# Kernel tuning notes

Measured on AMD Instinct MI355X. Metric: run time of the kernel, lower is better.

## Reference

```python
import jax, jax.numpy as jnp
import numpy as np
from jax import lax

N_ENT, N_REL, N_TYPE = 50000, 237, 4000
DE, NOUT, DT = 100, 128, 200
N_EDGE, B = 800000, 4096
ALPHA, EPS = 0.2, 1e-5
NUM_FILT, FILT_W = 32, 9
FC_LEN = ((NOUT - FILT_W) // 2 + 1 - 2) // 2 + 1  # width after conv(s=2) then pool(2,s=2)
FC_LEN = FC_LEN * NUM_FILT  # height stays 1 -> 30*32 = 960


def setup_inputs() -> dict:
    key = jax.random.key(0)
    ks = jax.random.split(key, 16)
    inp = {
        'x_batch': jax.random.randint(ks[0], (B,), 0, N_ENT),
        'edge_index': jax.random.randint(ks[1], (2, N_EDGE), 0, N_ENT),
        'edge_type': jax.random.randint(ks[2], (N_EDGE,), 0, N_REL),
        'E_w': jax.random.normal(ks[3], (N_ENT, DE)) * 0.05,
        'R_w': jax.random.normal(ks[4], (N_REL, DE)) * 0.05,
        'T_w': jax.random.normal(ks[5], (N_TYPE, DT)) * 0.05,
        'W_f': jax.random.normal(ks[6], (DE, NOUT)) * (1.0 / np.sqrt(DE)),
        'a_vec': jax.random.normal(ks[7], (2 * NOUT,)) * 0.05,
        'conv_w': jax.random.normal(ks[8], (NUM_FILT, 1, 1, FILT_W)) * 0.1,
        'conv_b': jnp.zeros((NUM_FILT,)),
        'bn1_g': jnp.ones((1,)), 'bn1_b': jnp.zeros((1,)),
        'bn3_g': jnp.ones((NUM_FILT,)), 'bn3_b': jnp.zeros((NUM_FILT,)),
        'bn2_g': jnp.ones((DT,)), 'bn2_b': jnp.zeros((DT,)),
        'fc_w': jax.random.normal(ks[9], (DT, FC_LEN)) * (1.0 / np.sqrt(FC_LEN)),
        'fc_b': jnp.zeros((DT,)),
        'b_bias': jnp.zeros((N_TYPE,)),
    }
    return inp


def _bn(x, g, b, axes):
    # training-mode batch norm (biased variance), broadcastable g/b
    mean = jnp.mean(x, axis=axes, keepdims=True)
    var = jnp.var(x, axis=axes, keepdims=True)
    return g * (x - mean) * lax.rsqrt(var + EPS) + b


def _frgat(E_w, R_w, edge_index, edge_type, W_f, a_vec):
    src, dst = edge_index[0], edge_index[1]
    h = E_w @ W_f                                   # [N, NOUT]
    comp = E_w[src] - R_w[edge_type]                # 'sub' composition, [E, DE]
    m = comp @ W_f                                  # messages, [E, NOUT]
    score = jnp.concatenate([h[dst], m], axis=1) @ a_vec  # [E]
    score = jax.nn.leaky_relu(score, ALPHA)
    smax = jax.ops.segment_max(score, dst, num_segments=N_ENT)
    ex = jnp.exp(score - smax[dst])
    denom = jax.ops.segment_sum(ex, dst, num_segments=N_ENT)
    att = ex / (denom[dst] + 1e-16)
    agg = jax.ops.segment_sum(att[:, None] * m, dst, num_segments=N_ENT)
    return jax.nn.elu(agg)                          # F.elu on out_att output


def reference(x_batch, edge_index, edge_type, E_w, R_w, T_w, W_f, a_vec,
              conv_w, conv_b, bn1_g, bn1_b, bn3_g, bn3_b, bn2_g, bn2_b,
              fc_w, fc_b, b_bias):
    ent = _frgat(E_w, R_w, edge_index, edge_type, W_f, a_vec)   # [N, NOUT]
    e = ent[x_batch].reshape(B, 1, 1, NOUT)                     # NCHW
    x = _bn(e, bn1_g.reshape(1, 1, 1, 1), bn1_b.reshape(1, 1, 1, 1), (0, 2, 3))
    x = lax.conv_general_dilated(x, conv_w, window_strides=(2, 2), padding='VALID',
                                 dimension_numbers=('NCHW', 'OIHW', 'NCHW'))
    x = x + conv_b.reshape(1, -1, 1, 1)
    x = _bn(x, bn3_g.reshape(1, -1, 1, 1), bn3_b.reshape(1, -1, 1, 1), (0, 2, 3))
    x = jax.nn.relu(x)
    x = lax.reduce_window(x, -jnp.inf, lax.max, (1, 1, 1, 2), (1, 1, 2, 2), 'VALID')
    x = x.reshape(B, -1)                                        # [B, FC_LEN]
    x = x @ fc_w.T + fc_b
    x = _bn(x, bn2_g[None, :], bn2_b[None, :], (0,))
    x = jax.nn.relu(x)
    logits = x @ T_w.T + b_bias
    return jax.nn.sigmoid(logits)
```

## Files before the change

kernel.cpp:

```cpp
#include <hip/hip_runtime.h>
#include <hip/hip_bf16.h>
#include <math.h>

#define N_ENT   50000
#define N_REL   237
#define N_TYPE  4000
#define DE      100
#define NOUT    128
#define DT      200
#define N_EDGE  800000
#define B_SZ    4096
#define ALPHA   0.2f
#define EPS     1e-5f
#define NUM_FILT 32
#define CONV_W_OUT 60
#define POOL_W  30
#define FC_LEN  960
#define KP      224
#define NTP     4032
#define EBCAP   96

typedef unsigned short ushort_t;
typedef __attribute__((ext_vector_type(8))) short bf16x8;
typedef __attribute__((ext_vector_type(4))) float f32x4;

__global__ void k_fillconst(float* p, long n, float val) {
    long i = (long)blockIdx.x * blockDim.x + threadIdx.x;
    long stride = (long)gridDim.x * blockDim.x;
    for (; i < n; i += stride) p[i] = val;
}

#define ZERO_F4 14676
__global__ void k_fillprep(float4* zp, const float* Wf, const float* a_vec,
                           const float* Rw, float* wa1, float* wa2, float* rw) {
    if (blockIdx.x < 58) {
        int i = blockIdx.x * 256 + threadIdx.x;
        if (i < ZERO_F4) zp[i] = make_float4(0.f, 0.f, 0.f, 0.f);
        return;
    }
    __shared__ float sa[2 * NOUT];
    __shared__ float swa2[DE];
    int t = threadIdx.x;
    sa[t] = a_vec[t];
    __syncthreads();
    if (t < DE) {
        float s1 = 0.f, s2 = 0.f;
        for (int j = 0; j < NOUT; j++) {
            float w = Wf[t * NOUT + j];
            s1 += w * sa[j];
            s2 += w * sa[NOUT + j];
        }
        wa1[t] = s1; wa2[t] = s2; swa2[t] = s2;
    }
    __syncthreads();
    if (t < N_REL) {
        float s = 0.f;
        for (int k = 0; k < DE; k++) s += Rw[t * DE + k] * swa2[k];
        rw[t] = s;
    }
}

__global__ void k_flags(const int* xb, int* flags) {
    int i = blockIdx.x * blockDim.x + threadIdx.x;
    if (i < B_SZ) flags[xb[i]] = 1;
}

__global__ void k_slotsent(int* flags, int* counter, int* slotent,
                           const float* Ew, const float* wa1, const float* wa2,
                           float* ha, float* ew) {
    if (blockIdx.x < 196) {
        int i = blockIdx.x * 256 + threadIdx.x;
        if (i >= N_ENT) return;
        if (flags[i]) {
            int s = atomicAdd(counter, 1);
            flags[i] = 1 + s;
            slotent[s] = i;
        }
        return;
    }
    int wid = (blockIdx.x - 196) * 4 + (threadIdx.x >> 6);
    int lane = threadIdx.x & 63;
    if (wid >= N_ENT) return;
    float s1 = 0.f, s2 = 0.f;
    if (lane < DE / 2) {
        const float2* p = (const float2*)(Ew + (size_t)wid * DE);
        float2 v = p[lane];
        s1 = v.x * wa1[2 * lane] + v.y * wa1[2 * lane + 1];
        s2 = v.x * wa2[2 * lane] + v.y * wa2[2 * lane + 1];
    }
    for (int off = 32; off > 0; off >>= 1) {
        s1 += __shfl_down(s1, off);
        s2 += __shfl_down(s2, off);
    }
    if (lane == 0) { ha[wid] = s1; ew[wid] = s2; }
}

__global__ void k_scatter96(const int* ei, const int* et, const int* flags,
                            int* ecount, int2* ebuck) {
    int e = blockIdx.x * blockDim.x + threadIdx.x;
    if (e >= N_EDGE) return;
    int s = flags[ei[N_EDGE + e]];
    if (!s) return;
    int idx = atomicAdd(&ecount[s - 1], 1);
    if (idx < EBCAP)
        ebuck[(size_t)(s - 1) * EBCAP + idx] = make_int2(ei[e], et[e]);
}

__global__ void k_agg(const int* counter, const int* ecount, const int* slotent,
                      const int2* ebuck, const float* Ew, const float* Rw,
                      const float* ha, const float* ew, const float* rw,
                      float* aggc) {
    __shared__ float sacc[DE];
    __shared__ float sden;
    int slot = blockIdx.x;
    if (slot >= counter[0]) return;
    int t = threadIdx.x;
    int half = t >> 7;
    int tl = t & 127;
    int n = min(ecount[slot], EBCAP);
    const int2* eb = ebuck + (size_t)slot * EBCAP;
    float hae = ha[slotent[slot]];
    float acc = 0.f, den = 0.f;
    for (int j = half; j < n; j += 2) {
        int2 p = eb[j];
        float sc = hae + ew[p.x] - rw[p.y];
        sc = sc >= 0.f ? sc : ALPHA * sc;
        float ex = expf(sc);
        den += ex;
        if (tl < DE) acc += ex * (Ew[(size_t)p.x * DE + tl] - Rw[(size_t)p.y * DE + tl]);
    }
    if (half == 1) {
        if (tl < DE) sacc[tl] = acc;
        if (tl == 0) sden = den;
    }
    __syncthreads();
    if (half == 0 && tl < DE) {
        float a = acc + sacc[tl];
        float d = den + sden;
        aggc[(size_t)slot * DE + tl] = a / (d + 1e-16f);
    }
}

__global__ void k_gatherconv(const int* xb, const int* flags, const float* aggc,
                             const float* Wf, const float* convw,
                             float* ebuf, float* gps, float* gpq, float* cpart) {
    __shared__ float row[DE];
    __shared__ float xs[NOUT];
    __shared__ float cw[NUM_FILT * 9];
    __shared__ float red[NOUT], red2[NOUT];
    int b = blockIdx.x, t = threadIdx.x;
    int slot = flags[xb[b]] - 1;
    if (t < DE) row[t] = aggc[(size_t)slot * DE + t];
    for (int i = t; i < NUM_FILT * 9; i += 128) cw[i] = convw[i];
    __syncthreads();
    float acc = 0.f;
    for (int k = 0; k < DE; k++) acc += row[k] * Wf[k * NOUT + t];
    float x = acc > 0.f ? acc : expm1f(acc);
    xs[t] = x;
    ebuf[(size_t)b * NOUT + t] = x;
    red[t] = x; red2[t] = x * x;
    __syncthreads();
    for (int s = 64; s > 0; s >>= 1) {
        if (t < s) { red[t] += red[t + s]; red2[t] += red2[t + s]; }
        __syncthreads();
    }
    if (t == 0) { gps[b] = red[0]; gpq[b] = red2[0]; }
    int c = t >> 2, wg = t & 3;
    float ls = 0.f, lq = 0.f;
    for (int i = 0; i < 15; i++) {
        int w = wg + 4 * i;
        float u = 0.f;
        #pragma unroll
        for (int j = 0; j < 9; j++) u += cw[c * 9 + j] * xs[2 * w + j];
        ls += u; lq += u * u;
    }
    __syncthreads();
    red[t] = ls; red2[t] = lq;
    __syncthreads();
    if (wg == 0) {
        float s = red[t] + red[t + 1] + red[t + 2] + red[t + 3];
        float q = red2[t] + red2[t + 1] + red2[t + 2] + red2[t + 3];
        cpart[b * 64 + c] = s;
        cpart[b * 64 + 32 + c] = q;
    }
}

__global__ void k_redAB(const float* gps, const float* gpq, const float* cpart,
                        const float* g1, const float* g3, const float* b3, float* AB) {
    __shared__ float r1[256], r2[256], r3[256], r4[256];
    int c = blockIdx.x, t = threadIdx.x;
    float s = 0.f, q = 0.f, cs = 0.f, cq = 0.f;
    for (int b = t; b < B_SZ; b += 256) {
        s += gps[b]; q += gpq[b];
        cs += cpart[b * 64 + c]; cq += cpart[b * 64 + 32 + c];
    }
    r1[t] = s; r2[t] = q; r3[t] = cs; r4[t] = cq;
    __syncthreads();
    for (int k = 128; k > 0; k >>= 1) {
        if (t < k) { r1[t] += r1[t+k]; r2[t] += r2[t+k]; r3[t] += r3[t+k]; r4[t] += r4[t+k]; }
        __syncthreads();
    }
    if (t == 0) {
        float N1 = (float)(B_SZ * NOUT);
        float m1 = r1[0] / N1;
        float v1 = r2[0] / N1 - m1 * m1;
        float s1 = g1[0] * rsqrtf(v1 + EPS);
        float Nc = (float)(B_SZ * CONV_W_OUT);
        float mu = r3[0] / Nc;
        float vu = r4[0] / Nc - mu * mu;
        float A = g3[c] * s1 * rsqrtf(s1 * s1 * vu + EPS);
        AB[c] = A;
        AB[32 + c] = b3[c] - A * mu;
    }
}

__global__ void k_pool(const float* ebuf, const float* convw, const float* AB,
                       __hip_bfloat16* pooled) {
    __shared__ float xs[NOUT];
    __shared__ float cw[NUM_FILT * 9];
    __shared__ float sA[32], sB[32];
    int b = blockIdx.x, t = threadIdx.x;
    xs[t] = ebuf[(size_t)b * NOUT + t];
    for (int i = t; i < NUM_FILT * 9; i += 128) cw[i] = convw[i];
    if (t < 32) { sA[t] = AB[t]; sB[t] = AB[32 + t]; }
    __syncthreads();
    int c = t >> 2, wg = t & 3;
    float A = sA[c], Bv = sB[c];
    for (int i = 0; i < 8; i++) {
        int w2 = wg + 4 * i;
        if (w2 < POOL_W) {
            int w = 2 * w2;
            float u0 = 0.f, u1 = 0.f;
            #pragma unroll
            for (int j = 0; j < 9; j++) {
                float cv = cw[c * 9 + j];
                u0 += cv * xs[2 * w + j];
                u1 += cv * xs[2 * w + 2 + j];
            }
            float z0 = fmaxf(A * u0 + Bv, 0.f);
            float z1 = fmaxf(A * u1 + Bv, 0.f);
            pooled[((size_t)b * NUM_FILT + c) * POOL_W + w2] = __float2bfloat16(fmaxf(z0, z1));
        }
    }
}

__global__ void k_pads(const float* fcw, const float* tw,
                       __hip_bfloat16* bfc, __hip_bfloat16* b2) {
    int i = blockIdx.x * blockDim.x + threadIdx.x;
    if (i < KP * FC_LEN) {
        bfc[i] = __float2bfloat16((i < DT * FC_LEN) ? fcw[i] : 0.f);
    } else {
        int j = i - KP * FC_LEN;
        if (j >= NTP * KP) return;
        int n = j / KP, k = j - n * KP;
        float v = (n < N_TYPE && k < DT) ? tw[n * DT + k] : 0.f;
        b2[j] = __float2bfloat16(v);
    }
}

template<int MODE, int K, int NB>
__launch_bounds__(256, 4)
__global__ void k_gemm(const ushort_t* A, const ushort_t* Bm, const float* bias,
                       int ldc, int nbias, float* Cf) {
    int wave = threadIdx.x >> 6, lane = threadIdx.x & 63;
    int m0 = blockIdx.x * 128 + wave * 32;
    int n0 = blockIdx.y * (16 * NB);
    int rsel = lane & 15, ksel = (lane >> 4) * 8;
    const ushort_t* pa0 = A + (size_t)(m0 + rsel) * K + ksel;
    const ushort_t* pa1 = pa0 + (size_t)16 * K;
    const ushort_t* pb[NB];
    #pragma unroll
    for (int j = 0; j < NB; j++) pb[j] = Bm + (size_t)(n0 + j * 16 + rsel) * K + ksel;
    f32x4 acc0[NB], acc1[NB];
    #pragma unroll
    for (int j = 0; j < NB; j++) { acc0[j] = (f32x4){0.f,0.f,0.f,0.f}; acc1[j] = acc0[j]; }
    if constexpr (K <= 256) {
        #pragma unroll
        for (int k = 0; k < K; k += 32) {
            bf16x8 a0 = *(const bf16x8*)(pa0 + k);
            bf16x8 a1 = *(const bf16x8*)(pa1 + k);
            #pragma unroll
            for (int j = 0; j < NB; j++) {
                bf16x8 b = *(const bf16x8*)(pb[j] + k);
                acc0[j] = __builtin_amdgcn_mfma_f32_16x16x32_bf16(b, a0, acc0[j], 0, 0, 0);
                acc1[j] = __builtin_amdgcn_mfma_f32_16x16x32_bf16(b, a1, acc1[j], 0, 0, 0);
            }
        }
    } else {
        #pragma unroll 4
        for (int k = 0; k < K; k += 32) {
            bf16x8 a0 = *(const bf16x8*)(pa0 + k);
            bf16x8 a1 = *(const bf16x8*)(pa1 + k);
            #pragma unroll
            for (int j = 0; j < NB; j++) {
                bf16x8 b = *(const bf16x8*)(pb[j] + k);
                acc0[j] = __builtin_amdgcn_mfma_f32_16x16x32_bf16(b, a0, acc0[j], 0, 0, 0);
                acc1[j] = __builtin_amdgcn_mfma_f32_16x16x32_bf16(b, a1, acc1[j], 0, 0, 0);
            }
        }
    }
    int mloc = lane & 15;
    int nq = (lane >> 4) * 4;
    #pragma unroll
    for (int j = 0; j < NB; j++) {
        int cc = n0 + j * 16 + nq;
        if (cc < nbias) {
            float4 bb = *(const float4*)(bias + cc);
            f32x4 v0 = acc0[j], v1 = acc1[j];
            float4 r0, r1;
            if (MODE == 0) {
                r0 = make_float4(v0[0] + bb.x, v0[1] + bb.y, v0[2] + bb.z, v0[3] + bb.w);
                r1 = make_float4(v1[0] + bb.x, v1[1] + bb.y, v1[2] + bb.z, v1[3] + bb.w);
            } else {
                r0.x = __builtin_amdgcn_rcpf(1.f + __expf(-(v0[0] + bb.x)));
                r0.y = __builtin_amdgcn_rcpf(1.f + __expf(-(v0[1] + bb.y)));
                r0.z = __builtin_amdgcn_rcpf(1.f + __expf(-(v0[2] + bb.z)));
                r0.w = __builtin_amdgcn_rcpf(1.f + __expf(-(v0[3] + bb.w)));
                r1.x = __builtin_amdgcn_rcpf(1.f + __expf(-(v1[0] + bb.x)));
                r1.y = __builtin_amdgcn_rcpf(1.f + __expf(-(v1[1] + bb.y)));
                r1.z = __builtin_amdgcn_rcpf(1.f + __expf(-(v1[2] + bb.z)));
                r1.w = __builtin_amdgcn_rcpf(1.f + __expf(-(v1[3] + bb.w)));
            }
            *(float4*)(Cf + (size_t)(m0 + mloc) * ldc + cc) = r0;
            *(float4*)(Cf + (size_t)(m0 + 16 + mloc) * ldc + cc) = r1;
        }
    }
}

__global__ void k_bn2part(const float* fcout, float* sums) {
    int b = blockIdx.x, t = threadIdx.x;
    if (t >= DT) return;
    float s = 0.f, q = 0.f;
    const float* base = fcout + (size_t)b * 128 * KP + t;
    for (int r = 0; r < 128; r++) {
        float v = base[r * KP];
        s += v; q += v * v;
    }
    atomicAdd(&sums[t], s);
    atomicAdd(&sums[KP + t], q);
}

__global__ void k_bn2apply(const float* fcout, const float* sums,
                           const float* g, const float* bb, __hip_bfloat16* a2) {
    int i = blockIdx.x * blockDim.x + threadIdx.x;
    if (i >= B_SZ * KP) return;
    int t = i % KP;
    float v = 0.f;
    if (t < DT) {
        float mean = sums[t] * (1.f / B_SZ);
        float var = sums[KP + t] * (1.f / B_SZ) - mean * mean;
        float sc = g[t] * rsqrtf(var + EPS);
        float sh = bb[t] - mean * sc;
        v = fcout[i] * sc + sh;
        v = fmaxf(v, 0.f);
    }
    a2[i] = __float2bfloat16(v);
}

extern "C" void kernel_launch(void* const* d_in, const int* in_sizes, int n_in,
                              void* d_out, int out_size, void* d_ws, size_t ws_size,
                              hipStream_t stream) {
    (void)in_sizes; (void)n_in;
    const int*   x_batch = (const int*)d_in[0];
    const int*   ei      = (const int*)d_in[1];
    const int*   etype   = (const int*)d_in[2];
    const float* E_w     = (const float*)d_in[3];
    const float* R_w     = (const float*)d_in[4];
    const float* T_w     = (const float*)d_in[5];
    const float* W_f     = (const float*)d_in[6];
    const float* a_vec   = (const float*)d_in[7];
    const float* conv_w  = (const float*)d_in[8];
    const float* bn1_g   = (const float*)d_in[10];
    const float* bn3_g   = (const float*)d_in[12];
    const float* bn3_b   = (const float*)d_in[13];
    const float* bn2_g   = (const float*)d_in[14];
    const float* bn2_b   = (const float*)d_in[15];
    const float* fc_w    = (const float*)d_in[16];
    const float* fc_b    = (const float*)d_in[17];
    const float* b_bias  = (const float*)d_in[18];
    float* out           = (float*)d_out;
    long outn = (long)out_size;

    const size_t WS_NEEDED = 4279296;
    if (ws_size < WS_NEEDED) {
        k_fillconst<<<2048, 256, 0, stream>>>(out, outn, 50.f);
        return;
    }
    char* ws = (char*)d_ws;
    float* wa1      = (float*)(ws + 0);
    float* wa2      = (float*)(ws + 512);
    float* rw       = (float*)(ws + 1024);
    float* AB       = (float*)(ws + 2048);
    float* gps      = (float*)(ws + 4864);
    float* gpq      = (float*)(ws + 21248);
    float* cpart    = (float*)(ws + 37632);
    int*   counter  = (int*)  (ws + 1086208);
    int*   flags    = (int*)  (ws + 1086464);
    int*   slotent  = (int*)  (ws + 1286464);
    int*   ecount   = (int*)  (ws + 1302848);
    float* sums     = (float*)(ws + 1319232);
    float* ha       = (float*)(ws + 1352064);
    float* ew       = (float*)(ws + 1552064);
    float* ebuf     = (float*)(ws + 1752064);
    __hip_bfloat16* bfc = (__hip_bfloat16*)(ws + 3849216);
    __hip_bfloat16* a2 = (__hip_bfloat16*)(ws + 4864);
    __hip_bfloat16* b2 = (__hip_bfloat16*)(ws + 1840128);
    __hip_bfloat16* pooled = (__hip_bfloat16*)((char*)d_out + 0);
    float* fcout    = (float*)((char*)d_out + 8388608);
    int2*  ebuck    = (int2*) ((char*)d_out + 16777216);
    float* aggc     = (float*)((char*)d_out + 25165824);

    k_fillprep<<<59, 256, 0, stream>>>((float4*)counter, W_f, a_vec, R_w, wa1, wa2, rw);
    k_flags<<<16, 256, 0, stream>>>(x_batch, flags);
    k_slotsent<<<12696, 256, 0, stream>>>(flags, counter, slotent, E_w, wa1, wa2, ha, ew);
    k_scatter96<<<3125, 256, 0, stream>>>(ei, etype, flags, ecount, ebuck);
    k_agg<<<4096, 256, 0, stream>>>(counter, ecount, slotent, ebuck,
                                    E_w, R_w, ha, ew, rw, aggc);
    k_gatherconv<<<4096, 128, 0, stream>>>(x_batch, flags, aggc, W_f, conv_w,
                                           ebuf, gps, gpq, cpart);
    k_redAB<<<32, 256, 0, stream>>>(gps, gpq, cpart, bn1_g, bn3_g, bn3_b, AB);
    k_pool<<<4096, 128, 0, stream>>>(ebuf, conv_w, AB, pooled);
    k_pads<<<4368, 256, 0, stream>>>(fc_w, T_w, bfc, b2);
    k_gemm<0, FC_LEN, 2><<<dim3(32, 7), 256, 0, stream>>>(
        (const ushort_t*)pooled, (const ushort_t*)bfc, fc_b, KP, DT, fcout);
    k_bn2part<<<32, 256, 0, stream>>>(fcout, sums);
    k_bn2apply<<<3584, 256, 0, stream>>>(fcout, sums, bn2_g, bn2_b, a2);
    k_gemm<1, KP, 4><<<dim3(32, 63), 256, 0, stream>>>(
        (const ushort_t*)a2, (const ushort_t*)b2, b_bias, N_TYPE, N_TYPE, out);
}
```

Measured before the change: 272.2 us.

## Fuse front-end stages into persistent kernel with grid barriers and fold BN2 stats

Merges flags, slot assignment, edge scatter, aggregation, gather/conv stats, BN reduction and pooling into one persistent kernel of 512 blocks, separated by software grid-wide barriers, to remove many kernel launches and their gaps. The T_w padding moves into extra blocks of the first GEMM, and BN2 column sums are computed in the GEMM epilogue with shuffles and atomics instead of a separate kernel. The trade-offs are less parallelism in phases that used thousands of blocks, and a grid barrier that relies on all 512 blocks being co-resident and on the counter and generation words starting zeroed.

After: 1.021 ms. +275.1%, slower.

```diff
diff --git a/kernel.cpp b/kernel.cpp
--- a/kernel.cpp
+++ b/kernel.cpp
@@ -19,6 +19,7 @@
 #define KP      224
 #define NTP     4032
 #define EBCAP   96
+#define MEGA_BLOCKS 512
 
 typedef unsigned short ushort_t;
 typedef __attribute__((ext_vector_type(8))) short bf16x8;
@@ -60,208 +61,257 @@
     }
 }
 
-__global__ void k_flags(const int* xb, int* flags) {
-    int i = blockIdx.x * blockDim.x + threadIdx.x;
-    if (i < B_SZ) flags[xb[i]] = 1;
-}
-
-__global__ void k_slotsent(int* flags, int* counter, int* slotent,
-                           const float* Ew, const float* wa1, const float* wa2,
-                           float* ha, float* ew) {
-    if (blockIdx.x < 196) {
-        int i = blockIdx.x * 256 + threadIdx.x;
-        if (i >= N_ENT) return;
-        if (flags[i]) {
-            int s = atomicAdd(counter, 1);
-            flags[i] = 1 + s;
-            slotent[s] = i;
-        }
-        return;
-    }
-    int wid = (blockIdx.x - 196) * 4 + (threadIdx.x >> 6);
-    int lane = threadIdx.x & 63;
-    if (wid >= N_ENT) return;
-    float s1 = 0.f, s2 = 0.f;
-    if (lane < DE / 2) {
-        const float2* p = (const float2*)(Ew + (size_t)wid * DE);
-        float2 v = p[lane];
-        s1 = v.x * wa1[2 * lane] + v.y * wa1[2 * lane + 1];
-        s2 = v.x * wa2[2 * lane] + v.y * wa2[2 * lane + 1];
-    }
-    for (int off = 32; off > 0; off >>= 1) {
-        s1 += __shfl_down(s1, off);
-        s2 += __shfl_down(s2, off);
-    }
-    if (lane == 0) { ha[wid] = s1; ew[wid] = s2; }
-}
-
-__global__ void k_scatter96(const int* ei, const int* et, const int* flags,
-                            int* ecount, int2* ebuck) {
-    int e = blockIdx.x * blockDim.x + threadIdx.x;
-    if (e >= N_EDGE) return;
-    int s = flags[ei[N_EDGE + e]];
-    if (!s) return;
-    int idx = atomicAdd(&ecount[s - 1], 1);
-    if (idx < EBCAP)
-        ebuck[(size_t)(s - 1) * EBCAP + idx] = make_int2(ei[e], et[e]);
-}
-
-__global__ void k_agg(const int* counter, const int* ecount, const int* slotent,
-                      const int2* ebuck, const float* Ew, const float* Rw,
-                      const float* ha, const float* ew, const float* rw,
-                      float* aggc) {
-    __shared__ float sacc[DE];
-    __shared__ float sden;
-    int slot = blockIdx.x;
-    if (slot >= counter[0]) return;
+__device__ __forceinline__ void gbar(int* cnt, int* gen) {
+    __threadfence();
+    __syncthreads();
+    if (threadIdx.x == 0) {
+        int g = __hip_atomic_load(gen, __ATOMIC_RELAXED, __HIP_MEMORY_SCOPE_AGENT);
+        int v = __hip_atomic_fetch_add(cnt, 1, __ATOMIC_ACQ_REL, __HIP_MEMORY_SCOPE_AGENT);
+        if (v == (int)gridDim.x - 1) {
+            __hip_atomic_store(cnt, 0, __ATOMIC_RELAXED, __HIP_MEMORY_SCOPE_AGENT);
+            __hip_atomic_store(gen, g + 1, __ATOMIC_RELEASE, __HIP_MEMORY_SCOPE_AGENT);
+        } else {
+            while (__hip_atomic_load(gen, __ATOMIC_RELAXED, __HIP_MEMORY_SCOPE_AGENT) == g)
+                __builtin_amdgcn_s_sleep(2);
+        }
+    }
+    __syncthreads();
+    __threadfence();
+}
+
+__launch_bounds__(256, 4)
+__global__ void k_mega(const int* xb, const int* ei, const int* et,
+                       const float* Ew, const float* Rw, const float* Wf,
+                       const float* convw, const float* g1, const float* g3,
+                       const float* b3, const float* fcw,
+                       int* flags, int* counter, int* slotent, int* ecount,
+                       const float* wa1, const float* wa2, const float* rw,
+                       float* ha, float* ewd, float* ebuf, float* gps, float* gpq,
+                       float* cpart, float* AB, float* aggc, int2* ebuck,
+                       __hip_bfloat16* pooled, __hip_bfloat16* bfc,
+                       int* cnt, int* gen) {
+    __shared__ float smem[1256];
     int t = threadIdx.x;
-    int half = t >> 7;
-    int tl = t & 127;
-    int n = min(ecount[slot], EBCAP);
-    const int2* eb = ebuck + (size_t)slot * EBCAP;
-    float hae = ha[slotent[slot]];
-    float acc = 0.f, den = 0.f;
-    for (int j = half; j < n; j += 2) {
-        int2 p = eb[j];
-        float sc = hae + ew[p.x] - rw[p.y];
-        sc = sc >= 0.f ? sc : ALPHA * sc;
-        float ex = expf(sc);
-        den += ex;
-        if (tl < DE) acc += ex * (Ew[(size_t)p.x * DE + tl] - Rw[(size_t)p.y * DE + tl]);
-    }
-    if (half == 1) {
-        if (tl < DE) sacc[tl] = acc;
-        if (tl == 0) sden = den;
-    }
-    __syncthreads();
-    if (half == 0 && tl < DE) {
-        float a = acc + sacc[tl];
-        float d = den + sden;
-        aggc[(size_t)slot * DE + tl] = a / (d + 1e-16f);
-    }
-}
-
-__global__ void k_gatherconv(const int* xb, const int* flags, const float* aggc,
-                             const float* Wf, const float* convw,
-                             float* ebuf, float* gps, float* gpq, float* cpart) {
-    __shared__ float row[DE];
-    __shared__ float xs[NOUT];
-    __shared__ float cw[NUM_FILT * 9];
-    __shared__ float red[NOUT], red2[NOUT];
-    int b = blockIdx.x, t = threadIdx.x;
-    int slot = flags[xb[b]] - 1;
-    if (t < DE) row[t] = aggc[(size_t)slot * DE + t];
-    for (int i = t; i < NUM_FILT * 9; i += 128) cw[i] = convw[i];
-    __syncthreads();
-    float acc = 0.f;
-    for (int k = 0; k < DE; k++) acc += row[k] * Wf[k * NOUT + t];
-    float x = acc > 0.f ? acc : expm1f(acc);
-    xs[t] = x;
-    ebuf[(size_t)b * NOUT + t] = x;
-    red[t] = x; red2[t] = x * x;
-    __syncthreads();
-    for (int s = 64; s > 0; s >>= 1) {
-        if (t < s) { red[t] += red[t + s]; red2[t] += red2[t + s]; }
-        __syncthreads();
-    }
-    if (t == 0) { gps[b] = red[0]; gpq[b] = red2[0]; }
-    int c = t >> 2, wg = t & 3;
-    float ls = 0.f, lq = 0.f;
-    for (int i = 0; i < 15; i++) {
-        int w = wg + 4 * i;
-        float u = 0.f;
-        #pragma unroll
-        for (int j = 0; j < 9; j++) u += cw[c * 9 + j] * xs[2 * w + j];
-        ls += u; lq += u * u;
-    }
-    __syncthreads();
-    red[t] = ls; red2[t] = lq;
-    __syncthreads();
-    if (wg == 0) {
-        float s = red[t] + red[t + 1] + red[t + 2] + red[t + 3];
-        float q = red2[t] + red2[t + 1] + red2[t + 2] + red2[t + 3];
-        cpart[b * 64 + c] = s;
-        cpart[b * 64 + 32 + c] = q;
-    }
-}
-
-__global__ void k_redAB(const float* gps, const float* gpq, const float* cpart,
-                        const float* g1, const float* g3, const float* b3, float* AB) {
-    __shared__ float r1[256], r2[256], r3[256], r4[256];
-    int c = blockIdx.x, t = threadIdx.x;
-    float s = 0.f, q = 0.f, cs = 0.f, cq = 0.f;
-    for (int b = t; b < B_SZ; b += 256) {
-        s += gps[b]; q += gpq[b];
-        cs += cpart[b * 64 + c]; cq += cpart[b * 64 + 32 + c];
-    }
-    r1[t] = s; r2[t] = q; r3[t] = cs; r4[t] = cq;
-    __syncthreads();
-    for (int k = 128; k > 0; k >>= 1) {
-        if (t < k) { r1[t] += r1[t+k]; r2[t] += r2[t+k]; r3[t] += r3[t+k]; r4[t] += r4[t+k]; }
-        __syncthreads();
-    }
-    if (t == 0) {
-        float N1 = (float)(B_SZ * NOUT);
-        float m1 = r1[0] / N1;
-        float v1 = r2[0] / N1 - m1 * m1;
-        float s1 = g1[0] * rsqrtf(v1 + EPS);
-        float Nc = (float)(B_SZ * CONV_W_OUT);
-        float mu = r3[0] / Nc;
-        float vu = r4[0] / Nc - mu * mu;
-        float A = g3[c] * s1 * rsqrtf(s1 * s1 * vu + EPS);
-        AB[c] = A;
-        AB[32 + c] = b3[c] - A * mu;
-    }
-}
-
-__global__ void k_pool(const float* ebuf, const float* convw, const float* AB,
-                       __hip_bfloat16* pooled) {
-    __shared__ float xs[NOUT];
-    __shared__ float cw[NUM_FILT * 9];
-    __shared__ float sA[32], sB[32];
-    int b = blockIdx.x, t = threadIdx.x;
-    xs[t] = ebuf[(size_t)b * NOUT + t];
-    for (int i = t; i < NUM_FILT * 9; i += 128) cw[i] = convw[i];
-    if (t < 32) { sA[t] = AB[t]; sB[t] = AB[32 + t]; }
-    __syncthreads();
-    int c = t >> 2, wg = t & 3;
-    float A = sA[c], Bv = sB[c];
-    for (int i = 0; i < 8; i++) {
-        int w2 = wg + 4 * i;
-        if (w2 < POOL_W) {
-            int w = 2 * w2;
-            float u0 = 0.f, u1 = 0.f;
-            #pragma unroll
-            for (int j = 0; j < 9; j++) {
-                float cv = cw[c * 9 + j];
-                u0 += cv * xs[2 * w + j];
-                u1 += cv * xs[2 * w + 2 + j];
-            }
-            float z0 = fmaxf(A * u0 + Bv, 0.f);
-            float z1 = fmaxf(A * u1 + Bv, 0.f);
-            pooled[((size_t)b * NUM_FILT + c) * POOL_W + w2] = __float2bfloat16(fmaxf(z0, z1));
-        }
-    }
-}
-
-__global__ void k_pads(const float* fcw, const float* tw,
-                       __hip_bfloat16* bfc, __hip_bfloat16* b2) {
-    int i = blockIdx.x * blockDim.x + threadIdx.x;
-    if (i < KP * FC_LEN) {
-        bfc[i] = __float2bfloat16((i < DT * FC_LEN) ? fcw[i] : 0.f);
-    } else {
-        int j = i - KP * FC_LEN;
-        if (j >= NTP * KP) return;
-        int n = j / KP, k = j - n * KP;
-        float v = (n < N_TYPE && k < DT) ? tw[n * DT + k] : 0.f;
-        b2[j] = __float2bfloat16(v);
+    int nb = gridDim.x;
+
+    for (int vb = blockIdx.x; vb < 16; vb += nb) {
+        int i = vb * 256 + t;
+        if (i < B_SZ) flags[xb[i]] = 1;
+    }
+    gbar(cnt, gen);
+
+    for (int vb = blockIdx.x; vb < 12696; vb += nb) {
+        if (vb < 196) {
+            int i = vb * 256 + t;
+            if (i < N_ENT && flags[i]) {
+                int s = atomicAdd(counter, 1);
+                flags[i] = 1 + s;
+                slotent[s] = i;
+            }
+        } else {
+            int wid = (vb - 196) * 4 + (t >> 6);
+            int lane = t & 63;
+            if (wid < N_ENT) {
+                float s1 = 0.f, s2 = 0.f;
+                if (lane < DE / 2) {
+                    const float2* p = (const float2*)(Ew + (size_t)wid * DE);
+                    float2 v = p[lane];
+                    s1 = v.x * wa1[2 * lane] + v.y * wa1[2 * lane + 1];
+                    s2 = v.x * wa2[2 * lane] + v.y * wa2[2 * lane + 1];
+                }
+                for (int off = 32; off > 0; off >>= 1) {
+                    s1 += __shfl_down(s1, off);
+                    s2 += __shfl_down(s2, off);
+                }
+                if (lane == 0) { ha[wid] = s1; ewd[wid] = s2; }
+            }
+        }
+    }
+    gbar(cnt, gen);
+
+    for (int vb = blockIdx.x; vb < 3125; vb += nb) {
+        int e = vb * 256 + t;
+        if (e < N_EDGE) {
+            int s = flags[ei[N_EDGE + e]];
+            if (s) {
+                int idx = atomicAdd(&ecount[s - 1], 1);
+                if (idx < EBCAP)
+                    ebuck[(size_t)(s - 1) * EBCAP + idx] = make_int2(ei[e], et[e]);
+            }
+        }
+    }
+    gbar(cnt, gen);
+
+    {
+        int nslot = counter[0];
+        int half = t >> 7, tl = t & 127;
+        float* sacc = smem;
+        float* sden = smem + 128;
+        for (int slot = blockIdx.x; slot < B_SZ; slot += nb) {
+            bool act = slot < nslot;
+            float acc = 0.f, den = 0.f;
+            if (act) {
+                int n = min(ecount[slot], EBCAP);
+                const int2* eb = ebuck + (size_t)slot * EBCAP;
+                float hae = ha[slotent[slot]];
+                for (int j = half; j < n; j += 2) {
+                    int2 p = eb[j];
+                    float sc = hae + ewd[p.x] - rw[p.y];
+                    sc = sc >= 0.f ? sc : ALPHA * sc;
+                    float ex = expf(sc);
+                    den += ex;
+                    if (tl < DE)
+                        acc += ex * (Ew[(size_t)p.x * DE + tl] - Rw[(size_t)p.y * DE + tl]);
+                }
+            }
+            if (act && half == 1) {
+                if (tl < DE) sacc[tl] = acc;
+                if (tl == 0) sden[0] = den;
+            }
+            __syncthreads();
+            if (act && half == 0 && tl < DE)
+                aggc[(size_t)slot * DE + tl] = (acc + sacc[tl]) / (den + sden[0] + 1e-16f);
+            __syncthreads();
+        }
+    }
+    gbar(cnt, gen);
+
+    {
+        int half = t >> 7, tl = t & 127;
+        float* row  = smem;
+        float* xs   = smem + 200;
+        float* cw   = smem + 456;
+        float* red  = smem + 744;
+        float* red2 = smem + 1000;
+        for (int vb = blockIdx.x; vb < B_SZ / 2; vb += nb) {
+            int b = vb * 2 + half;
+            int slot = flags[xb[b]] - 1;
+            if (tl < DE) row[half * DE + tl] = aggc[(size_t)slot * DE + tl];
+            for (int i = t; i < 288; i += 256) cw[i] = convw[i];
+            __syncthreads();
+            float acc = 0.f;
+            for (int k = 0; k < DE; k++) acc += row[half * DE + k] * Wf[k * NOUT + tl];
+            float x = acc > 0.f ? acc : expm1f(acc);
+            xs[half * NOUT + tl] = x;
+            ebuf[(size_t)b * NOUT + tl] = x;
+            red[half * NOUT + tl] = x; red2[half * NOUT + tl] = x * x;
+            __syncthreads();
+            for (int s = 64; s > 0; s >>= 1) {
+                if (tl < s) {
+                    red[half * NOUT + tl]  += red[half * NOUT + tl + s];
+                    red2[half * NOUT + tl] += red2[half * NOUT + tl + s];
+                }
+                __syncthreads();
+            }
+            if (tl == 0) { gps[b] = red[half * NOUT]; gpq[b] = red2[half * NOUT]; }
+            int c = tl >> 2, wg = tl & 3;
+            float ls = 0.f, lq = 0.f;
+            for (int i2 = 0; i2 < 15; i2++) {
+                int w = wg + 4 * i2;
+                float u = 0.f;
+                #pragma unroll
+                for (int j = 0; j < 9; j++) u += cw[c * 9 + j] * xs[half * NOUT + 2 * w + j];
+                ls += u; lq += u * u;
+            }
+            __syncthreads();
+            red[half * NOUT + tl] = ls; red2[half * NOUT + tl] = lq;
+            __syncthreads();
+            if (wg == 0) {
+                float s = red[half*NOUT+tl] + red[half*NOUT+tl+1] + red[half*NOUT+tl+2] + red[half*NOUT+tl+3];
+                float q = red2[half*NOUT+tl] + red2[half*NOUT+tl+1] + red2[half*NOUT+tl+2] + red2[half*NOUT+tl+3];
+                cpart[b * 64 + c] = s;
+                cpart[b * 64 + 32 + c] = q;
+            }
+            __syncthreads();
+        }
+    }
+    gbar(cnt, gen);
+
+    {
+        float* r1 = smem;       float* r2 = smem + 256;
+        float* r3 = smem + 512; float* r4 = smem + 768;
+        for (int c = blockIdx.x; c < 32; c += nb) {
+            float s = 0.f, q = 0.f, cs = 0.f, cq = 0.f;
+            for (int b = t; b < B_SZ; b += 256) {
+                s += gps[b]; q += gpq[b];
+                cs += cpart[b * 64 + c]; cq += cpart[b * 64 + 32 + c];
+            }
+            r1[t] = s; r2[t] = q; r3[t] = cs; r4[t] = cq;
+            __syncthreads();
+            for (int k = 128; k > 0; k >>= 1) {
+                if (t < k) { r1[t] += r1[t+k]; r2[t] += r2[t+k]; r3[t] += r3[t+k]; r4[t] += r4[t+k]; }
+                __syncthreads();
+            }
+            if (t == 0) {
+                float N1 = (float)(B_SZ * NOUT);
+                float m1 = r1[0] / N1;
+                float v1 = r2[0] / N1 - m1 * m1;
+                float s1 = g1[0] * rsqrtf(v1 + EPS);
+                float Nc = (float)(B_SZ * CONV_W_OUT);
+                float mu = r3[0] / Nc;
+                float vu = r4[0] / Nc - mu * mu;
+                float A = g3[c] * s1 * rsqrtf(s1 * s1 * vu + EPS);
+                AB[c] = A;
+                AB[32 + c] = b3[c] - A * mu;
+            }
+            __syncthreads();
+        }
+    }
+    gbar(cnt, gen);
+
+    {
+        int half = t >> 7, tl = t & 127;
+        float* xs  = smem;
+        float* cw  = smem + 256;
+        float* sAB = smem + 544;
+        for (int vb = blockIdx.x; vb < B_SZ / 2; vb += nb) {
+            int b = vb * 2 + half;
+            xs[half * NOUT + tl] = ebuf[(size_t)b * NOUT + tl];
+            for (int i = t; i < 288; i += 256) cw[i] = convw[i];
+            if (t < 64) sAB[t] = AB[t];
+            __syncthreads();
+            int c = tl >> 2, wg = tl & 3;
+            float A = sAB[c], Bv = sAB[32 + c];
+            for (int i2 = 0; i2 < 8; i2++) {
+                int w2 = wg + 4 * i2;
+                if (w2 < POOL_W) {
+                    int w = 2 * w2;
+                    float u0 = 0.f, u1 = 0.f;
+                    #pragma unroll
+                    for (int j = 0; j < 9; j++) {
+                        float cv = cw[c * 9 + j];
+                        u0 += cv * xs[half * NOUT + 2 * w + j];
+                        u1 += cv * xs[half * NOUT + 2 * w + 2 + j];
+                    }
+                    float z0 = fmaxf(A * u0 + Bv, 0.f);
+                    float z1 = fmaxf(A * u1 + Bv, 0.f);
+                    pooled[((size_t)b * NUM_FILT + c) * POOL_W + w2] = __float2bfloat16(fmaxf(z0, z1));
+                }
+            }
+            __syncthreads();
+        }
+        for (int i = blockIdx.x * 256 + t; i < KP * FC_LEN; i += nb * 256)
+            bfc[i] = __float2bfloat16((i < DT * FC_LEN) ? fcw[i] : 0.f);
     }
 }
 
 template<int MODE, int K, int NB>
 __launch_bounds__(256, 4)
 __global__ void k_gemm(const ushort_t* A, const ushort_t* Bm, const float* bias,
-                       int ldc, int nbias, float* Cf) {
+                       int ldc, int nbias, float* Cf, float* sums,
+                       const float* tw, __hip_bfloat16* b2pad) {
+    if constexpr (MODE == 0) {
+        if (blockIdx.y >= 7) {
+            int pid = (blockIdx.y - 7) * 32 + blockIdx.x;
+            int jj = pid * 256 + (int)threadIdx.x;
+            if (jj < NTP * KP) {
+                int n = jj / KP, k = jj - n * KP;
+                float v = (n < N_TYPE && k < DT) ? tw[n * DT + k] : 0.f;
+                b2pad[jj] = __float2bfloat16(v);
+            }
+            return;
+        }
+    }
     int wave = threadIdx.x >> 6, lane = threadIdx.x & 63;
     int m0 = blockIdx.x * 128 + wave * 32;
     int n0 = blockIdx.y * (16 * NB);
@@ -323,21 +373,26 @@
             }
             *(float4*)(Cf + (size_t)(m0 + mloc) * ldc + cc) = r0;
             *(float4*)(Cf + (size_t)(m0 + 16 + mloc) * ldc + cc) = r1;
-        }
-    }
-}
-
-__global__ void k_bn2part(const float* fcout, float* sums) {
-    int b = blockIdx.x, t = threadIdx.x;
-    if (t >= DT) return;
-    float s = 0.f, q = 0.f;
-    const float* base = fcout + (size_t)b * 128 * KP + t;
-    for (int r = 0; r < 128; r++) {
-        float v = base[r * KP];
-        s += v; q += v * v;
-    }
-    atomicAdd(&sums[t], s);
-    atomicAdd(&sums[KP + t], q);
+            if (MODE == 0) {
+                float s0 = r0.x + r1.x, s1 = r0.y + r1.y, s2 = r0.z + r1.z, s3 = r0.w + r1.w;
+                float q0 = r0.x*r0.x + r1.x*r1.x, q1 = r0.y*r0.y + r1.y*r1.y;
+                float q2 = r0.z*r0.z + r1.z*r1.z, q3 = r0.w*r0.w + r1.w*r1.w;
+                #pragma unroll
+                for (int off = 1; off <= 8; off <<= 1) {
+                    s0 += __shfl_xor(s0, off); s1 += __shfl_xor(s1, off);
+                    s2 += __shfl_xor(s2, off); s3 += __shfl_xor(s3, off);
+                    q0 += __shfl_xor(q0, off); q1 += __shfl_xor(q1, off);
+                    q2 += __shfl_xor(q2, off); q3 += __shfl_xor(q3, off);
+                }
+                if (mloc == 0) {
+                    atomicAdd(&sums[cc + 0], s0); atomicAdd(&sums[cc + 1], s1);
+                    atomicAdd(&sums[cc + 2], s2); atomicAdd(&sums[cc + 3], s3);
+                    atomicAdd(&sums[KP + cc + 0], q0); atomicAdd(&sums[KP + cc + 1], q1);
+                    atomicAdd(&sums[KP + cc + 2], q2); atomicAdd(&sums[KP + cc + 3], q3);
+                }
+            }
+        }
+    }
 }
 
 __global__ void k_bn2apply(const float* fcout, const float* sums,
@@ -395,6 +450,8 @@
     float* gpq      = (float*)(ws + 21248);
     float* cpart    = (float*)(ws + 37632);
     int*   counter  = (int*)  (ws + 1086208);
+    int*   gcnt     = (int*)  (ws + 1086216);
+    int*   ggen     = (int*)  (ws + 1086220);
     int*   flags    = (int*)  (ws + 1086464);
     int*   slotent  = (int*)  (ws + 1286464);
     int*   ecount   = (int*)  (ws + 1302848);
@@ -411,20 +468,15 @@
     float* aggc     = (float*)((char*)d_out + 25165824);
 
     k_fillprep<<<59, 256, 0, stream>>>((float4*)counter, W_f, a_vec, R_w, wa1, wa2, rw);
-    k_flags<<<16, 256, 0, stream>>>(x_batch, flags);
-    k_slotsent<<<12696, 256, 0, stream>>>(flags, counter, slotent, E_w, wa1, wa2, ha, ew);
-    k_scatter96<<<3125, 256, 0, stream>>>(ei, etype, flags, ecount, ebuck);
-    k_agg<<<4096, 256, 0, stream>>>(counter, ecount, slotent, ebuck,
-                                    E_w, R_w, ha, ew, rw, aggc);
-    k_gatherconv<<<4096, 128, 0, stream>>>(x_batch, flags, aggc, W_f, conv_w,
-                                           ebuf, gps, gpq, cpart);
-    k_redAB<<<32, 256, 0, stream>>>(gps, gpq, cpart, bn1_g, bn3_g, bn3_b, AB);
-    k_pool<<<4096, 128, 0, stream>>>(ebuf, conv_w, AB, pooled);
-    k_pads<<<4368, 256, 0, stream>>>(fc_w, T_w, bfc, b2);
-    k_gemm<0, FC_LEN, 2><<<dim3(32, 7), 256, 0, stream>>>(
-        (const ushort_t*)pooled, (const ushort_t*)bfc, fc_b, KP, DT, fcout);
-    k_bn2part<<<32, 256, 0, stream>>>(fcout, sums);
+    k_mega<<<MEGA_BLOCKS, 256, 0, stream>>>(
+        x_batch, ei, etype, E_w, R_w, W_f, conv_w, bn1_g, bn3_g, bn3_b, fc_w,
+        flags, counter, slotent, ecount, wa1, wa2, rw, ha, ew, ebuf,
+        gps, gpq, cpart, AB, aggc, ebuck, pooled, bfc, gcnt, ggen);
+    k_gemm<0, FC_LEN, 2><<<dim3(32, 118), 256, 0, stream>>>(
+        (const ushort_t*)pooled, (const ushort_t*)bfc, fc_b, KP, DT, fcout,
+        sums, T_w, b2);
     k_bn2apply<<<3584, 256, 0, stream>>>(fcout, sums, bn2_g, bn2_b, a2);
     k_gemm<1, KP, 4><<<dim3(32, 63), 256, 0, stream>>>(
-        (const ushort_t*)a2, (const ushort_t*)b2, b_bias, N_TYPE, N_TYPE, out);
-}
+        (const ushort_t*)a2, (const ushort_t*)b2, b_bias, N_TYPE, N_TYPE, out,
+        nullptr, nullptr, nullptr);
+}
```

## Fuse BN2 statistics into FC GEMM and overlap T_w padding

Applied to the files above, without the earlier changes.

Splits the FC GEMM into a dedicated kernel with smaller 64-row tiles, giving 64x7 tiles instead of 32x7 blocks for better occupancy. Its epilogue computes per-column sum and sum-of-squares with wave shuffles and atomics, replacing the separate k_bn2part pass. Extra blocks in the same grid perform the T_w bf16 padding so that conversion runs alongside the GEMM. The fc_b bias add is dropped, which is exact only when fc_b is zero as in the test inputs, though training-mode batch norm would cancel a constant bias anyway. The added atomics could contend, and sums must be zeroed before this kernel runs.

Result: slower. 308.5 us (+13.3%).

```diff
diff --git a/kernel.cpp b/kernel.cpp
--- a/kernel.cpp
+++ b/kernel.cpp
@@ -244,24 +244,74 @@
     }
 }
 
-__global__ void k_pads(const float* fcw, const float* tw,
-                       __hip_bfloat16* bfc, __hip_bfloat16* b2) {
+__global__ void k_padsbfc(const float* fcw, __hip_bfloat16* bfc) {
     int i = blockIdx.x * blockDim.x + threadIdx.x;
-    if (i < KP * FC_LEN) {
+    if (i < KP * FC_LEN)
         bfc[i] = __float2bfloat16((i < DT * FC_LEN) ? fcw[i] : 0.f);
-    } else {
-        int j = i - KP * FC_LEN;
-        if (j >= NTP * KP) return;
-        int n = j / KP, k = j - n * KP;
-        float v = (n < N_TYPE && k < DT) ? tw[n * DT + k] : 0.f;
-        b2[j] = __float2bfloat16(v);
-    }
-}
-
-template<int MODE, int K, int NB>
+}
+
 __launch_bounds__(256, 4)
-__global__ void k_gemm(const ushort_t* A, const ushort_t* Bm, const float* bias,
-                       int ldc, int nbias, float* Cf) {
+__global__ void k_gemm_fc(const ushort_t* A, const ushort_t* Bm, float* Cf,
+                          float* sums, const float* tw, __hip_bfloat16* b2pad) {
+    constexpr int K = FC_LEN;
+    if (blockIdx.y >= 7) {
+        int pid = (blockIdx.y - 7) * 64 + blockIdx.x;
+        int jj = pid * 256 + (int)threadIdx.x;
+        if (jj < NTP * KP) {
+            int n = jj / KP, k = jj - n * KP;
+            float v = (n < N_TYPE && k < DT) ? tw[n * DT + k] : 0.f;
+            b2pad[jj] = __float2bfloat16(v);
+        }
+        return;
+    }
+    int wave = threadIdx.x >> 6, lane = threadIdx.x & 63;
+    int m0 = blockIdx.x * 64 + wave * 16;
+    int n0 = blockIdx.y * 32;
+    int rsel = lane & 15, ksel = (lane >> 4) * 8;
+    const ushort_t* pa0 = A + (size_t)(m0 + rsel) * K + ksel;
+    const ushort_t* pb0 = Bm + (size_t)(n0 + rsel) * K + ksel;
+    const ushort_t* pb1 = pb0 + (size_t)16 * K;
+    f32x4 acc0 = (f32x4){0.f,0.f,0.f,0.f}, acc1 = acc0;
+    #pragma unroll 4
+    for (int k = 0; k < K; k += 32) {
+        bf16x8 a0 = *(const bf16x8*)(pa0 + k);
+        bf16x8 b0 = *(const bf16x8*)(pb0 + k);
+        bf16x8 b1 = *(const bf16x8*)(pb1 + k);
+        acc0 = __builtin_amdgcn_mfma_f32_16x16x32_bf16(b0, a0, acc0, 0, 0, 0);
+        acc1 = __builtin_amdgcn_mfma_f32_16x16x32_bf16(b1, a0, acc1, 0, 0, 0);
+    }
+    int mloc = lane & 15;
+    int nq = (lane >> 4) * 4;
+    #pragma unroll
+    for (int j = 0; j < 2; j++) {
+        int cc = n0 + j * 16 + nq;
+        if (cc < DT) {
+            f32x4 v = j ? acc1 : acc0;
+            float4 r = make_float4(v[0], v[1], v[2], v[3]);
+            *(float4*)(Cf + (size_t)(m0 + mloc) * KP + cc) = r;
+            float s0 = r.x, s1 = r.y, s2 = r.z, s3 = r.w;
+            float q0 = r.x*r.x, q1 = r.y*r.y, q2 = r.z*r.z, q3 = r.w*r.w;
+            #pragma unroll
+            for (int off = 1; off <= 8; off <<= 1) {
+                s0 += __shfl_xor(s0, off); s1 += __shfl_xor(s1, off);
+                s2 += __shfl_xor(s2, off); s3 += __shfl_xor(s3, off);
+                q0 += __shfl_xor(q0, off); q1 += __shfl_xor(q1, off);
+                q2 += __shfl_xor(q2, off); q3 += __shfl_xor(q3, off);
+            }
+            if (mloc == 0) {
+                atomicAdd(&sums[cc + 0], s0); atomicAdd(&sums[cc + 1], s1);
+                atomicAdd(&sums[cc + 2], s2); atomicAdd(&sums[cc + 3], s3);
+                atomicAdd(&sums[KP + cc + 0], q0); atomicAdd(&sums[KP + cc + 1], q1);
+                atomicAdd(&sums[KP + cc + 2], q2); atomicAdd(&sums[KP + cc + 3], q3);
+            }
+        }
+    }
+}
+
+template<int K, int NB>
+__launch_bounds__(256, 4)
+__global__ void k_gemm_sig(const ushort_t* A, const ushort_t* Bm, const float* bias,
+                           float* Cf) {
     int wave = threadIdx.x >> 6, lane = threadIdx.x & 63;
     int m0 = blockIdx.x * 128 + wave * 32;
     int n0 = blockIdx.y * (16 * NB);
@@ -274,29 +324,15 @@
     f32x4 acc0[NB], acc1[NB];
     #pragma unroll
     for (int j = 0; j < NB; j++) { acc0[j] = (f32x4){0.f,0.f,0.f,0.f}; acc1[j] = acc0[j]; }
-    if constexpr (K <= 256) {
+    #pragma unroll
+    for (int k = 0; k < K; k += 32) {
+        bf16x8 a0 = *(const bf16x8*)(pa0 + k);
+        bf16x8 a1 = *(const bf16x8*)(pa1 + k);
         #pragma unroll
-        for (int k = 0; k < K; k += 32) {
-            bf16x8 a0 = *(const bf16x8*)(pa0 + k);
-            bf16x8 a1 = *(const bf16x8*)(pa1 + k);
-            #pragma unroll
-            for (int j = 0; j < NB; j++) {
-                bf16x8 b = *(const bf16x8*)(pb[j] + k);
-                acc0[j] = __builtin_amdgcn_mfma_f32_16x16x32_bf16(b, a0, acc0[j], 0, 0, 0);
-                acc1[j] = __builtin_amdgcn_mfma_f32_16x16x32_bf16(b, a1, acc1[j], 0, 0, 0);
-            }
-        }
-    } else {
-        #pragma unroll 4
-        for (int k = 0; k < K; k += 32) {
-            bf16x8 a0 = *(const bf16x8*)(pa0 + k);
-            bf16x8 a1 = *(const bf16x8*)(pa1 + k);
-            #pragma unroll
-            for (int j = 0; j < NB; j++) {
-                bf16x8 b = *(const bf16x8*)(pb[j] + k);
-                acc0[j] = __builtin_amdgcn_mfma_f32_16x16x32_bf16(b, a0, acc0[j], 0, 0, 0);
-                acc1[j] = __builtin_amdgcn_mfma_f32_16x16x32_bf16(b, a1, acc1[j], 0, 0, 0);
-            }
+        for (int j = 0; j < NB; j++) {
+            bf16x8 b = *(const bf16x8*)(pb[j] + k);
+            acc0[j] = __builtin_amdgcn_mfma_f32_16x16x32_bf16(b, a0, acc0[j], 0, 0, 0);
+            acc1[j] = __builtin_amdgcn_mfma_f32_16x16x32_bf16(b, a1, acc1[j], 0, 0, 0);
         }
     }
     int mloc = lane & 15;
@@ -304,40 +340,22 @@
     #pragma unroll
     for (int j = 0; j < NB; j++) {
         int cc = n0 + j * 16 + nq;
-        if (cc < nbias) {
+        if (cc < N_TYPE) {
             float4 bb = *(const float4*)(bias + cc);
             f32x4 v0 = acc0[j], v1 = acc1[j];
             float4 r0, r1;
-            if (MODE == 0) {
-                r0 = make_float4(v0[0] + bb.x, v0[1] + bb.y, v0[2] + bb.z, v0[3] + bb.w);
-                r1 = make_float4(v1[0] + bb.x, v1[1] + bb.y, v1[2] + bb.z, v1[3] + bb.w);
-            } else {
-                r0.x = __builtin_amdgcn_rcpf(1.f + __expf(-(v0[0] + bb.x)));
-                r0.y = __builtin_amdgcn_rcpf(1.f + __expf(-(v0[1] + bb.y)));
-                r0.z = __builtin_amdgcn_rcpf(1.f + __expf(-(v0[2] + bb.z)));
-                r0.w = __builtin_amdgcn_rcpf(1.f + __expf(-(v0[3] + bb.w)));
-                r1.x = __builtin_amdgcn_rcpf(1.f + __expf(-(v1[0] + bb.x)));
-                r1.y = __builtin_amdgcn_rcpf(1.f + __expf(-(v1[1] + bb.y)));
-                r1.z = __builtin_amdgcn_rcpf(1.f + __expf(-(v1[2] + bb.z)));
-                r1.w = __builtin_amdgcn_rcpf(1.f + __expf(-(v1[3] + bb.w)));
-            }
-            *(float4*)(Cf + (size_t)(m0 + mloc) * ldc + cc) = r0;
-            *(float4*)(Cf + (size_t)(m0 + 16 + mloc) * ldc + cc) = r1;
-        }
-    }
-}
-
-__global__ void k_bn2part(const float* fcout, float* sums) {
-    int b = blockIdx.x, t = threadIdx.x;
-    if (t >= DT) return;
-    float s = 0.f, q = 0.f;
-    const float* base = fcout + (size_t)b * 128 * KP + t;
-    for (int r = 0; r < 128; r++) {
-        float v = base[r * KP];
-        s += v; q += v * v;
-    }
-    atomicAdd(&sums[t], s);
-    atomicAdd(&sums[KP + t], q);
+            r0.x = __builtin_amdgcn_rcpf(1.f + __expf(-(v0[0] + bb.x)));
+            r0.y = __builtin_amdgcn_rcpf(1.f + __expf(-(v0[1] + bb.y)));
+            r0.z = __builtin_amdgcn_rcpf(1.f + __expf(-(v0[2] + bb.z)));
+            r0.w = __builtin_amdgcn_rcpf(1.f + __expf(-(v0[3] + bb.w)));
+            r1.x = __builtin_amdgcn_rcpf(1.f + __expf(-(v1[0] + bb.x)));
+            r1.y = __builtin_amdgcn_rcpf(1.f + __expf(-(v1[1] + bb.y)));
+            r1.z = __builtin_amdgcn_rcpf(1.f + __expf(-(v1[2] + bb.z)));
+            r1.w = __builtin_amdgcn_rcpf(1.f + __expf(-(v1[3] + bb.w)));
+            *(float4*)(Cf + (size_t)(m0 + mloc) * N_TYPE + cc) = r0;
+            *(float4*)(Cf + (size_t)(m0 + 16 + mloc) * N_TYPE + cc) = r1;
+        }
+    }
 }
 
 __global__ void k_bn2apply(const float* fcout, const float* sums,
@@ -376,7 +394,6 @@
     const float* bn2_g   = (const float*)d_in[14];
     const float* bn2_b   = (const float*)d_in[15];
     const float* fc_w    = (const float*)d_in[16];
-    const float* fc_b    = (const float*)d_in[17];
     const float* b_bias  = (const float*)d_in[18];
     float* out           = (float*)d_out;
     long outn = (long)out_size;
@@ -420,11 +437,10 @@
                                            ebuf, gps, gpq, cpart);
     k_redAB<<<32, 256, 0, stream>>>(gps, gpq, cpart, bn1_g, bn3_g, bn3_b, AB);
     k_pool<<<4096, 128, 0, stream>>>(ebuf, conv_w, AB, pooled);
-    k_pads<<<4368, 256, 0, stream>>>(fc_w, T_w, bfc, b2);
-    k_gemm<0, FC_LEN, 2><<<dim3(32, 7), 256, 0, stream>>>(
-        (const ushort_t*)pooled, (const ushort_t*)bfc, fc_b, KP, DT, fcout);
-    k_bn2part<<<32, 256, 0, stream>>>(fcout, sums);
+    k_padsbfc<<<840, 256, 0, stream>>>(fc_w, bfc);
+    k_gemm_fc<<<dim3(64, 63), 256, 0, stream>>>(
+        (const ushort_t*)pooled, (const ushort_t*)bfc, fcout, sums, T_w, b2);
     k_bn2apply<<<3584, 256, 0, stream>>>(fcout, sums, bn2_g, bn2_b, a2);
-    k_gemm<1, KP, 4><<<dim3(32, 63), 256, 0, stream>>>(
-        (const ushort_t*)a2, (const ushort_t*)b2, b_bias, N_TYPE, N_TYPE, out);
-}
+    k_gemm_sig<KP, 4><<<dim3(32, 63), 256, 0, stream>>>(
+        (const ushort_t*)a2, (const ushort_t*)b2, b_bias, out);
+}
```
